# Kernel tuning notes

Hardware: AMD Instinct MI355X
Metric: run time of the kernel (lower is better)

## Reference

```python
import jax, jax.numpy as jnp
import numpy as np

B, T, C = 8, 1024, 1024
H, D = 16, 64  # num_heads, head_size

def setup_inputs() -> dict:
    key = jax.random.key(0)
    ks = jax.random.split(key, 6)
    s = C ** -0.5
    return {
        "x": jax.random.normal(ks[0], (B, T, C), dtype=jnp.float32),
        "Wq": jax.random.normal(ks[1], (H, C, D), dtype=jnp.float32) * s,
        "Wk": jax.random.normal(ks[2], (H, C, D), dtype=jnp.float32) * s,
        "Wv": jax.random.normal(ks[3], (H, C, D), dtype=jnp.float32) * s,
        "Wproj": jax.random.normal(ks[4], (H * D, C), dtype=jnp.float32) * ((H * D) ** -0.5),
        "bproj": jnp.zeros((C,), dtype=jnp.float32),
    }

def reference(x, Wq, Wk, Wv, Wproj, bproj):
    # per-head QKV projections, batched over heads via einsum (same math as looped heads)
    q = jnp.einsum('btc,hcd->bhtd', x, Wq)
    k = jnp.einsum('btc,hcd->bhtd', x, Wk)
    v = jnp.einsum('btc,hcd->bhtd', x, Wv)
    scale = D ** -0.5  # k.shape[-1]**-0.5 in original head
    scores = jnp.einsum('bhtd,bhsd->bhts', q, k) * scale  # [B,H,T,T]
    Tn = x.shape[1]
    causal = jnp.tril(jnp.ones((Tn, Tn), dtype=bool))
    scores = jnp.where(causal, scores, jnp.float32(-jnp.inf))
    att = jax.nn.softmax(scores, axis=-1)
    out = jnp.einsum('bhts,bhsd->bhtd', att, v)          # [B,H,T,D]
    out = out.transpose(0, 2, 1, 3).reshape(x.shape[0], Tn, H * D)  # concat heads
    return out @ Wproj + bproj  # dropout is identity at p=0.0
```

## Files before the change

### kernel.cpp

```cpp
#include <hip/hip_runtime.h>
#include <hip/hip_bf16.h>

#define B_ 8
#define T_ 1024
#define C_ 1024
#define H_ 16
#define D_ 64
#define QKVLD 3072

typedef short v4s __attribute__((ext_vector_type(4)));
typedef short v8s __attribute__((ext_vector_type(8)));
typedef float v4f __attribute__((ext_vector_type(4)));
typedef float v16f __attribute__((ext_vector_type(16)));

__device__ __forceinline__ unsigned short f2b(float f) {
    unsigned int u = __builtin_bit_cast(unsigned int, f);
    unsigned int lsb = (u >> 16) & 1u;
    u += 0x7fffu + lsb;
    return (unsigned short)(u >> 16);
}

__device__ __forceinline__ v4s pack4(float p0, float p1, float p2, float p3) {
    unsigned int a = (__builtin_bit_cast(unsigned int, p0) + 0x8000u) >> 16;
    unsigned int b = (__builtin_bit_cast(unsigned int, p1) + 0x8000u) & 0xFFFF0000u;
    unsigned int c = (__builtin_bit_cast(unsigned int, p2) + 0x8000u) >> 16;
    unsigned int d = (__builtin_bit_cast(unsigned int, p3) + 0x8000u) & 0xFFFF0000u;
    union { unsigned int u[2]; v4s v; } t;
    t.u[0] = a | b; t.u[1] = c | d;
    return t.v;
}

#define MFMA32(A, B, C) __builtin_amdgcn_mfma_f32_16x16x32_bf16(A, B, C, 0, 0, 0)
#define MFMA16(A, B, C) __builtin_amdgcn_mfma_f32_16x16x16bf16_1k(A, B, C, 0, 0, 0)

#define GLOAD16(gp, lp)                                                          \
    __builtin_amdgcn_global_load_lds(                                            \
        (const __attribute__((address_space(1))) unsigned int*)(gp),             \
        (__attribute__((address_space(3))) unsigned int*)(lp), 16, 0, 0)

__global__ void prep_kernel(const float* __restrict__ x, const float* __restrict__ Wq,
                            const float* __restrict__ Wk, const float* __restrict__ Wv,
                            const float* __restrict__ Wproj,
                            unsigned short* __restrict__ xb,
                            unsigned short* __restrict__ WqkvT,
                            unsigned short* __restrict__ WprojT) {
    __shared__ unsigned short t[64][65];
    int g = blockIdx.x;
    if (g < 8192) {
        int i = (g * 256 + (int)threadIdx.x) * 4;
        float4 v = *(const float4*)(x + i);
        ushort4 o;
        o.x = f2b(v.x); o.y = f2b(v.y); o.z = f2b(v.z); o.w = f2b(v.w);
        *(ushort4*)(xb + i) = o;
    } else if (g < 8192 + 768) {
        int idx = g - 8192;
        int z = idx >> 4;
        int h = z / 3, part = z % 3;
        const float* src = (part == 0 ? Wq : (part == 1 ? Wk : Wv)) + (size_t)h * C_ * D_;
        int c0 = (idx & 15) * 64;
        for (int i = threadIdx.x; i < 4096; i += 256) {
            int r = i >> 6, d = i & 63;
            t[d][r] = f2b(src[(size_t)(c0 + r) * D_ + d]);
        }
        __syncthreads();
        unsigned short* dst = WqkvT + (size_t)(part * 1024 + h * 64) * C_;
        for (int i = threadIdx.x; i < 4096; i += 256) {
            int d = i >> 6, r = i & 63;
            dst[(size_t)d * C_ + c0 + r] = t[d][r];
        }
    } else {
        int idx = g - 8960;
        int n0 = (idx & 15) * 64, k0 = (idx >> 4) * 64;
        for (int i = threadIdx.x; i < 4096; i += 256) {
            int r = i >> 6, c = i & 63;
            t[c][r] = f2b(Wproj[(size_t)(k0 + r) * C_ + n0 + c]);
        }
        __syncthreads();
        for (int i = threadIdx.x; i < 4096; i += 256) {
            int n = i >> 6, k = i & 63;
            WprojT[(size_t)(n0 + n) * 1024 + k0 + k] = t[n][k];
        }
    }
}

__global__ __launch_bounds__(256, 2) void gemm_qkv(const unsigned short* __restrict__ A,
                                                   const unsigned short* __restrict__ Bt,
                                                   unsigned short* __restrict__ Cout,
                                                   unsigned short* __restrict__ Vt,
                                                   int K, int ldc) {
    __shared__ unsigned short smem[24576];

    int tid = threadIdx.x;
    int lane = tid & 63, w = tid >> 6;
    int half = lane >> 5, l32 = lane & 31;
    int wm = w >> 1, wn = w & 1;
    int g = blockIdx.x;
    int xcd = g & 7;
    int bank = g >> 3;
    int j = g >> 4;

    if ((bank & 1) == 0) {
        constexpr int ABUF = 256 * 32;
        constexpr int BBUF = 128 * 32;
        unsigned short* lA0 = smem;
        unsigned short* lB0 = smem + 2 * ABUF;

        int m0 = (xcd * 4 + (j & 3)) * 256;
        int n0 = (j >> 2) * 128;

        const unsigned short* gA[4];
        int offA[4];
        #pragma unroll
        for (int jj = 0; jj < 4; jj++) {
            int c = jj * 256 + tid;
            int row = c >> 2;
            int col8 = ((c & 3) ^ ((row >> 1) & 3)) * 8;
            gA[jj] = A + (size_t)(m0 + row) * K + col8;
            offA[jj] = (jj * 256 + w * 64) * 16;
        }
        const unsigned short* gB[2];
        int offB[2];
        #pragma unroll
        for (int jj = 0; jj < 2; jj++) {
            int c = jj * 256 + tid;
            int row = c >> 2;
            int col8 = ((c & 3) ^ ((row >> 1) & 3)) * 8;
            gB[jj] = Bt + (size_t)(n0 + row) * K + col8;
            offB[jj] = (jj * 256 + w * 64) * 16;
        }

        int am[4], bn[2];
        #pragma unroll
        for (int mi = 0; mi < 4; mi++) am[mi] = wm * 128 + mi * 32 + l32;
        #pragma unroll
        for (int ni = 0; ni < 2; ni++) bn[ni] = wn * 64 + ni * 32 + l32;

        v16f acc[4][2];
        #pragma unroll
        for (int mi = 0; mi < 4; mi++)
            #pragma unroll
            for (int ni = 0; ni < 2; ni++)
                #pragma unroll
                for (int r = 0; r < 16; r++) acc[mi][ni][r] = 0.f;

        int ktiles = K >> 5;
        #pragma unroll
        for (int jj = 0; jj < 4; jj++) GLOAD16(gA[jj], (char*)lA0 + offA[jj]);
        #pragma unroll
        for (int jj = 0; jj < 2; jj++) GLOAD16(gB[jj], (char*)lB0 + offB[jj]);

        for (int it = 0; it < ktiles; it++) {
            int cur = it & 1, nxt = cur ^ 1;
            __asm__ volatile("s_waitcnt vmcnt(0)" ::: "memory");
            __asm__ volatile("s_barrier" ::: "memory");
            {
                int kn = (it + 1 < ktiles) ? (it + 1) * 32 : it * 32;
                #pragma unroll
                for (int jj = 0; jj < 4; jj++) GLOAD16(gA[jj] + kn, (char*)(lA0 + nxt * ABUF) + offA[jj]);
                #pragma unroll
                for (int jj = 0; jj < 2; jj++) GLOAD16(gB[jj] + kn, (char*)(lB0 + nxt * BBUF) + offB[jj]);
            }
            const unsigned short* bufA = lA0 + cur * ABUF;
            const unsigned short* bufB = lB0 + cur * BBUF;
            #pragma unroll
            for (int step = 0; step < 2; step++) {
                int gc = step * 2 + half;
                v8s af[4], bf[2];
                #pragma unroll
                for (int mi = 0; mi < 4; mi++)
                    af[mi] = *(const v8s*)&bufA[am[mi] * 32 + ((gc ^ ((am[mi] >> 1) & 3)) * 8)];
                #pragma unroll
                for (int ni = 0; ni < 2; ni++)
                    bf[ni] = *(const v8s*)&bufB[bn[ni] * 32 + ((gc ^ ((bn[ni] >> 1) & 3)) * 8)];
                #pragma unroll
                for (int mi = 0; mi < 4; mi++)
                    #pragma unroll
                    for (int ni = 0; ni < 2; ni++)
                        acc[mi][ni] = __builtin_amdgcn_mfma_f32_32x32x16_bf16(af[mi], bf[ni], acc[mi][ni], 0, 0, 0);
            }
        }
        float scl = (n0 >= 1024) ? 0.125f : 1.0f;
        #pragma unroll
        for (int mi = 0; mi < 4; mi++) {
            #pragma unroll
            for (int ni = 0; ni < 2; ni++) {
                int col = n0 + wn * 64 + ni * 32 + l32;
                #pragma unroll
                for (int r = 0; r < 16; r++) {
                    int row = m0 + wm * 128 + mi * 32 + (r & 3) + 8 * (r >> 2) + 4 * half;
                    Cout[(size_t)row * ldc + col] = f2b(acc[mi][ni][r] * scl);
                }
            }
        }
    } else {
        constexpr int ABUF = 128 * 32;
        constexpr int BBUF = 128 * 32;
        unsigned short* lA = smem;
        unsigned short* lB = smem + 3 * ABUF;

        const unsigned short* Bv = Bt + (size_t)2048 * K;
        int m0 = (xcd * 8 + (j & 7)) * 128;
        int n0 = (j >> 3) * 128;

        const unsigned short* gA[2];
        int offA[2];
        #pragma unroll
        for (int jj = 0; jj < 2; jj++) {
            int c = jj * 256 + tid;
            int row = c >> 2;
            int col8 = ((c & 3) ^ ((row >> 1) & 3)) * 8;
            gA[jj] = A + (size_t)(m0 + row) * K + col8;
            offA[jj] = (jj * 256 + w * 64) * 16;
        }
        const unsigned short* gB[2];
        int offB[2];
        #pragma unroll
        for (int jj = 0; jj < 2; jj++) {
            int c = jj * 256 + tid;
            int row = c >> 2;
            int col8 = ((c & 3) ^ ((row >> 1) & 3)) * 8;
            gB[jj] = Bv + (size_t)(n0 + row) * K + col8;
            offB[jj] = (jj * 256 + w * 64) * 16;
        }

        int am[2], bn[2];
        #pragma unroll
        for (int mi = 0; mi < 2; mi++) am[mi] = wm * 64 + mi * 32 + l32;
        #pragma unroll
        for (int ni = 0; ni < 2; ni++) bn[ni] = wn * 64 + ni * 32 + l32;

        v16f acc[2][2];
        #pragma unroll
        for (int mi = 0; mi < 2; mi++)
            #pragma unroll
            for (int ni = 0; ni < 2; ni++)
                #pragma unroll
                for (int r = 0; r < 16; r++) acc[mi][ni][r] = 0.f;

        int kt = K >> 5;
        #pragma unroll
        for (int jj = 0; jj < 2; jj++) GLOAD16(gA[jj], (char*)lA + offA[jj]);
        #pragma unroll
        for (int jj = 0; jj < 2; jj++) GLOAD16(gB[jj], (char*)lB + offB[jj]);
        #pragma unroll
        for (int jj = 0; jj < 2; jj++) GLOAD16(gA[jj] + 32, (char*)(lA + ABUF) + offA[jj]);
        #pragma unroll
        for (int jj = 0; jj < 2; jj++) GLOAD16(gB[jj] + 32, (char*)(lB + BBUF) + offB[jj]);

        int cur = 0;
        for (int it = 0; it < kt; it++) {
            int nx2 = cur + 2; if (nx2 >= 3) nx2 -= 3;
            __asm__ volatile("s_waitcnt vmcnt(4)" ::: "memory");
            __asm__ volatile("s_barrier" ::: "memory");
            {
                int kn = ((it + 2 < kt) ? it + 2 : kt - 1) << 5;
                #pragma unroll
                for (int jj = 0; jj < 2; jj++) GLOAD16(gA[jj] + kn, (char*)(lA + nx2 * ABUF) + offA[jj]);
                #pragma unroll
                for (int jj = 0; jj < 2; jj++) GLOAD16(gB[jj] + kn, (char*)(lB + nx2 * BBUF) + offB[jj]);
            }
            const unsigned short* bufA = lA + cur * ABUF;
            const unsigned short* bufB = lB + cur * BBUF;
            #pragma unroll
            for (int step = 0; step < 2; step++) {
                int gch = step * 2 + half;
                v8s af[2], bf[2];
                #pragma unroll
                for (int mi = 0; mi < 2; mi++)
                    af[mi] = *(const v8s*)&bufA[am[mi] * 32 + ((gch ^ ((am[mi] >> 1) & 3)) * 8)];
                #pragma unroll
                for (int ni = 0; ni < 2; ni++)
                    bf[ni] = *(const v8s*)&bufB[bn[ni] * 32 + ((gch ^ ((bn[ni] >> 1) & 3)) * 8)];
                #pragma unroll
                for (int mi = 0; mi < 2; mi++)
                    #pragma unroll
                    for (int ni = 0; ni < 2; ni++)
                        acc[mi][ni] = __builtin_amdgcn_mfma_f32_32x32x16_bf16(af[mi], bf[ni], acc[mi][ni], 0, 0, 0);
            }
            cur = cur + 1; if (cur >= 3) cur -= 3;
        }
        unsigned short* sT = lA;
        int bB = m0 >> 10;
        int t0 = m0 & 1023;
        #pragma unroll
        for (int p = 0; p < 2; p++) {
            __syncthreads();
            if (wn == p) {
                #pragma unroll
                for (int mi = 0; mi < 2; mi++)
                    #pragma unroll
                    for (int ni = 0; ni < 2; ni++) {
                        int cl = ni * 32 + l32;
                        #pragma unroll
                        for (int r = 0; r < 16; r++) {
                            int rowl = wm * 64 + mi * 32 + (r & 3) + 8 * (r >> 2) + 4 * half;
                            sT[cl * 136 + rowl] = f2b(acc[mi][ni][r]);
                        }
                    }
            }
            __syncthreads();
            #pragma unroll
            for (int jj = 0; jj < 4; jj++) {
                int c = jj * 256 + tid;
                int cl = c >> 4, ch = c & 15;
                int vcol = n0 + p * 64 + cl;
                int hh = vcol >> 6, dd = vcol & 63;
                *(v8s*)&Vt[(((size_t)bB * 16 + hh) * 64 + dd) * T_ + t0 + ch * 8] =
                    *(const v8s*)&sT[cl * 136 + ch * 8];
            }
        }
    }
}

__global__ __launch_bounds__(256, 3) void gemm_proj(const unsigned short* __restrict__ A,
                                                    const unsigned short* __restrict__ Bt,
                                                    float* __restrict__ Cout,
                                                    const float* __restrict__ bias,
                                                    int M, int N, int K) {
    constexpr int ABUF = 128 * 32;
    constexpr int BBUF = 128 * 32;
    __shared__ unsigned short lA[3 * ABUF];
    __shared__ unsigned short lB[3 * BBUF];

    int tid = threadIdx.x;
    int lane = tid & 63, w = tid >> 6;
    int half = lane >> 5, l32 = lane & 31;
    int wm = w >> 1, wn = w & 1;

    int g = blockIdx.x;
    int nbm = M / 128;
    int stripe = nbm >> 3;
    int xcd = g & 7, s = g >> 3;
    int m0 = (xcd * stripe + (s % stripe)) * 128;
    int n0 = (s / stripe) * 128;

    const unsigned short* gA[2];
    int offA[2];
    #pragma unroll
    for (int j = 0; j < 2; j++) {
        int c = j * 256 + tid;
        int row = c >> 2;
        int col8 = ((c & 3) ^ ((row >> 1) & 3)) * 8;
        gA[j] = A + (size_t)(m0 + row) * K + col8;
        offA[j] = (j * 256 + w * 64) * 16;
    }
    const unsigned short* gB[2];
    int offB[2];
    #pragma unroll
    for (int j = 0; j < 2; j++) {
        int c = j * 256 + tid;
        int row = c >> 2;
        int col8 = ((c & 3) ^ ((row >> 1) & 3)) * 8;
        gB[j] = Bt + (size_t)(n0 + row) * K + col8;
        offB[j] = (j * 256 + w * 64) * 16;
    }

    int am[2], bn[2];
    #pragma unroll
    for (int mi = 0; mi < 2; mi++) am[mi] = wm * 64 + mi * 32 + l32;
    #pragma unroll
    for (int ni = 0; ni < 2; ni++) bn[ni] = wn * 64 + ni * 32 + l32;

    v16f acc[2][2];
    #pragma unroll
    for (int mi = 0; mi < 2; mi++)
        #pragma unroll
        for (int ni = 0; ni < 2; ni++)
            #pragma unroll
            for (int r = 0; r < 16; r++) acc[mi][ni][r] = 0.f;

    int kt = K >> 5;
    #pragma unroll
    for (int j = 0; j < 2; j++) GLOAD16(gA[j], (char*)lA + offA[j]);
    #pragma unroll
    for (int j = 0; j < 2; j++) GLOAD16(gB[j], (char*)lB + offB[j]);
    #pragma unroll
    for (int j = 0; j < 2; j++) GLOAD16(gA[j] + 32, (char*)(lA + ABUF) + offA[j]);
    #pragma unroll
    for (int j = 0; j < 2; j++) GLOAD16(gB[j] + 32, (char*)(lB + BBUF) + offB[j]);

    int cur = 0;
    for (int it = 0; it < kt; it++) {
        int nx2 = cur + 2; if (nx2 >= 3) nx2 -= 3;
        __asm__ volatile("s_waitcnt vmcnt(4)" ::: "memory");
        __asm__ volatile("s_barrier" ::: "memory");
        {
            int kn = ((it + 2 < kt) ? it + 2 : kt - 1) << 5;
            #pragma unroll
            for (int j = 0; j < 2; j++) GLOAD16(gA[j] + kn, (char*)(lA + nx2 * ABUF) + offA[j]);
            #pragma unroll
            for (int j = 0; j < 2; j++) GLOAD16(gB[j] + kn, (char*)(lB + nx2 * BBUF) + offB[j]);
        }
        const unsigned short* bufA = lA + cur * ABUF;
        const unsigned short* bufB = lB + cur * BBUF;
        #pragma unroll
        for (int step = 0; step < 2; step++) {
            int gch = step * 2 + half;
            v8s af[2], bf[2];
            #pragma unroll
            for (int mi = 0; mi < 2; mi++)
                af[mi] = *(const v8s*)&bufA[am[mi] * 32 + ((gch ^ ((am[mi] >> 1) & 3)) * 8)];
            #pragma unroll
            for (int ni = 0; ni < 2; ni++)
                bf[ni] = *(const v8s*)&bufB[bn[ni] * 32 + ((gch ^ ((bn[ni] >> 1) & 3)) * 8)];
            #pragma unroll
            for (int mi = 0; mi < 2; mi++)
                #pragma unroll
                for (int ni = 0; ni < 2; ni++)
                    acc[mi][ni] = __builtin_amdgcn_mfma_f32_32x32x16_bf16(af[mi], bf[ni], acc[mi][ni], 0, 0, 0);
        }
        cur = cur + 1; if (cur >= 3) cur -= 3;
    }
    #pragma unroll
    for (int mi = 0; mi < 2; mi++) {
        #pragma unroll
        for (int ni = 0; ni < 2; ni++) {
            int col = n0 + wn * 64 + ni * 32 + l32;
            #pragma unroll
            for (int r = 0; r < 16; r++) {
                int row = m0 + wm * 64 + mi * 32 + (r & 3) + 8 * (r >> 2) + 4 * half;
                Cout[(size_t)row * N + col] = acc[mi][ni][r] + bias[col];
            }
        }
    }
}

__global__ __launch_bounds__(256) void attn_kernel(const unsigned short* __restrict__ QKV,
                                                   const unsigned short* __restrict__ Vt,
                                                   unsigned short* __restrict__ Ob) {
    int bh = blockIdx.x;
    int qt = 15 - blockIdx.y;
    int b = bh >> 4, h = bh & 15;
    int tid = threadIdx.x, lane = tid & 63, w = tid >> 6;
    int quad = lane >> 4, l16 = lane & 15;
    int qg0 = qt * 64 + w * 16;

    __shared__ unsigned short lK[2][2][64][32];
    __shared__ unsigned short lV[2][2][64][32];

    v8s aq0, aq1;
    {
        const unsigned short* qp = QKV + (size_t)(b * T_ + qg0 + l16) * QKVLD + h * 64;
        aq0 = *(const v8s*)(qp + quad * 8);
        aq1 = *(const v8s*)(qp + 32 + quad * 8);
    }

    const unsigned short* gK[2];
    const unsigned short* gV[2];
    int ldsOff[2];
    #pragma unroll
    for (int j = 0; j < 2; j++) {
        int c = j * 256 + tid;
        int halfp = c >> 8, row = (c >> 2) & 63;
        int col8 = ((c & 3) ^ ((row >> 1) & 3)) * 8;
        gK[j] = QKV + (size_t)(b * T_ + row) * QKVLD + 1024 + h * 64 + halfp * 32 + col8;
        gV[j] = Vt + ((size_t)bh * 64 + row) * T_ + halfp * 32 + col8;
        ldsOff[j] = (j * 256 + w * 64) * 16;
    }
    int rcol = (quad ^ ((l16 >> 1) & 3)) * 8;

    v4f accO[4];
    float lsum = 0.f;
    #pragma unroll
    for (int i = 0; i < 4; i++) accO[i] = (v4f){0.f, 0.f, 0.f, 0.f};

    int ntiles = qt + 1;

    #pragma unroll
    for (int j = 0; j < 2; j++) GLOAD16(gK[j], (char*)&lK[0][0][0][0] + ldsOff[j]);
    #pragma unroll
    for (int j = 0; j < 2; j++) GLOAD16(gV[j], (char*)&lV[0][0][0][0] + ldsOff[j]);

    for (int it = 0; it < ntiles; it++) {
        int cur = it & 1, nxt = cur ^ 1;
        int s0 = it * 64;
        __asm__ volatile("s_waitcnt vmcnt(0)" ::: "memory");
        __asm__ volatile("s_barrier" ::: "memory");
        {
            int itn = (it + 1 < ntiles) ? it + 1 : it;
            size_t koff = (size_t)itn * 64 * QKVLD;
            #pragma unroll
            for (int j = 0; j < 2; j++)
                GLOAD16(gK[j] + koff, (char*)&lK[nxt][0][0][0] + ldsOff[j]);
            size_t voff = (size_t)itn * 64;
            #pragma unroll
            for (int j = 0; j < 2; j++)
                GLOAD16(gV[j] + voff, (char*)&lV[nxt][0][0][0] + ldsOff[j]);
        }
        v4f sf[4];
        #pragma unroll
        for (int nt = 0; nt < 4; nt++) {
            v8s bk0 = *(const v8s*)&lK[cur][0][nt * 16 + l16][rcol];
            v8s bk1 = *(const v8s*)&lK[cur][1][nt * 16 + l16][rcol];
            v4f a = (v4f){0.f, 0.f, 0.f, 0.f};
            a = MFMA32(bk0, aq0, a);
            a = MFMA32(bk1, aq1, a);
            sf[nt] = a;
        }
        bool diag = (it == ntiles - 1);
        int qg = qg0 + l16;
        v4s pP[4];
        #pragma unroll
        for (int nt = 0; nt < 4; nt++) {
            float p[4];
            #pragma unroll
            for (int r = 0; r < 4; r++) {
                float e = __expf(sf[nt][r]);
                if (diag) {
                    int sg = s0 + nt * 16 + quad * 4 + r;
                    e = (sg > qg) ? 0.f : e;
                }
                p[r] = e;
                lsum += e;
            }
            pP[nt] = pack4(p[0], p[1], p[2], p[3]);
        }
        #pragma unroll
        for (int kb = 0; kb < 4; kb++) {
            int sc_ = kb >> 1;
            int ccg = (kb & 1) * 2 + (quad >> 1);
            #pragma unroll
            for (int dt = 0; dt < 4; dt++) {
                int d = dt * 16 + l16;
                int ccp = ccg ^ ((l16 >> 1) & 3);
                v4s bv = *(const v4s*)&lV[cur][sc_][d][ccp * 8 + (quad & 1) * 4];
                accO[dt] = MFMA16(pP[kb], bv, accO[dt]);
            }
        }
    }
    float ls = lsum;
    ls += __shfl_xor(ls, 16, 64);
    ls += __shfl_xor(ls, 32, 64);
    #pragma unroll
    for (int r = 0; r < 4; r++) {
        float lq = __shfl(ls, quad * 4 + r, 64);
        float inv = 1.0f / lq;
        int q = qg0 + quad * 4 + r;
        #pragma unroll
        for (int dt = 0; dt < 4; dt++) {
            int d = dt * 16 + l16;
            Ob[(size_t)(b * T_ + q) * (H_ * D_) + h * 64 + d] = f2b(accO[dt][r] * inv);
        }
    }
}

extern "C" void kernel_launch(void* const* d_in, const int* in_sizes, int n_in,
                              void* d_out, int out_size, void* d_ws, size_t ws_size,
                              hipStream_t stream) {
    const float* x     = (const float*)d_in[0];
    const float* Wq    = (const float*)d_in[1];
    const float* Wk    = (const float*)d_in[2];
    const float* Wv    = (const float*)d_in[3];
    const float* Wproj = (const float*)d_in[4];
    const float* bproj = (const float*)d_in[5];
    float* out = (float*)d_out;

    char* ws = (char*)d_ws;
    unsigned short* xb     = (unsigned short*)ws;
    unsigned short* WqkvT  = (unsigned short*)(ws + 16777216);
    unsigned short* WprojT = (unsigned short*)(ws + 23068672);
    unsigned short* QKV    = (unsigned short*)(ws + 25165824);
    unsigned short* Vt     = (unsigned short*)(ws + 75497472);
    unsigned short* Ob     = (unsigned short*)(ws + 92274688);

    prep_kernel<<<dim3(9216), dim3(256), 0, stream>>>(x, Wq, Wk, Wv, Wproj, xb, WqkvT, WprojT);
    gemm_qkv<<<dim3(1024), dim3(256), 0, stream>>>(xb, WqkvT, QKV, Vt, 1024, QKVLD);
    attn_kernel<<<dim3(128, 16), dim3(256), 0, stream>>>(QKV, Vt, Ob);
    gemm_proj<<<dim3(512), dim3(256), 0, stream>>>(Ob, WprojT, out, bproj, 8192, 1024, 1024);
}
```

Baseline: 230.9 us.

## Process 128 query rows per attention block to reuse K/V tiles across two subtiles

Each attention workgroup now handles 128 query rows instead of 64, with each wave computing two 16-row subtiles that share the same K and V fragments read from LDS. This halves the grid along the query axis and halves the global K/V traffic and LDS reads per query row. In exchange it raises register pressure (two accumulator sets), lowers block count and parallelism, and wastes some work on the two diagonal tiles where masking now spans a wider region.

```diff
diff --git a/kernel.cpp b/kernel.cpp
--- a/kernel.cpp
+++ b/kernel.cpp
@@ -429,20 +429,21 @@
                                                    const unsigned short* __restrict__ Vt,
                                                    unsigned short* __restrict__ Ob) {
     int bh = blockIdx.x;
-    int qt = 15 - blockIdx.y;
+    int qt = 7 - blockIdx.y;
     int b = bh >> 4, h = bh & 15;
     int tid = threadIdx.x, lane = tid & 63, w = tid >> 6;
     int quad = lane >> 4, l16 = lane & 15;
-    int qg0 = qt * 64 + w * 16;
+    int qg0 = qt * 128 + w * 32;
 
     __shared__ unsigned short lK[2][2][64][32];
     __shared__ unsigned short lV[2][2][64][32];
 
-    v8s aq0, aq1;
-    {
-        const unsigned short* qp = QKV + (size_t)(b * T_ + qg0 + l16) * QKVLD + h * 64;
-        aq0 = *(const v8s*)(qp + quad * 8);
-        aq1 = *(const v8s*)(qp + 32 + quad * 8);
+    v8s aq[2][2];
+    #pragma unroll
+    for (int st = 0; st < 2; st++) {
+        const unsigned short* qp = QKV + (size_t)(b * T_ + qg0 + st * 16 + l16) * QKVLD + h * 64;
+        aq[st][0] = *(const v8s*)(qp + quad * 8);
+        aq[st][1] = *(const v8s*)(qp + 32 + quad * 8);
     }
 
     const unsigned short* gK[2];
@@ -459,12 +460,14 @@
     }
     int rcol = (quad ^ ((l16 >> 1) & 3)) * 8;
 
-    v4f accO[4];
-    float lsum = 0.f;
-    #pragma unroll
-    for (int i = 0; i < 4; i++) accO[i] = (v4f){0.f, 0.f, 0.f, 0.f};
-
-    int ntiles = qt + 1;
+    v4f accO[2][4];
+    float lsum[2] = {0.f, 0.f};
+    #pragma unroll
+    for (int st = 0; st < 2; st++)
+        #pragma unroll
+        for (int i = 0; i < 4; i++) accO[st][i] = (v4f){0.f, 0.f, 0.f, 0.f};
+
+    int ntiles = 2 * qt + 2;
 
     #pragma unroll
     for (int j = 0; j < 2; j++) GLOAD16(gK[j], (char*)&lK[0][0][0][0] + ldsOff[j]);
@@ -487,33 +490,31 @@
             for (int j = 0; j < 2; j++)
                 GLOAD16(gV[j] + voff, (char*)&lV[nxt][0][0][0] + ldsOff[j]);
         }
-        v4f sf[4];
+        bool diag = (it >= ntiles - 2);
+        v4s pP[2][4];
         #pragma unroll
         for (int nt = 0; nt < 4; nt++) {
             v8s bk0 = *(const v8s*)&lK[cur][0][nt * 16 + l16][rcol];
             v8s bk1 = *(const v8s*)&lK[cur][1][nt * 16 + l16][rcol];
-            v4f a = (v4f){0.f, 0.f, 0.f, 0.f};
-            a = MFMA32(bk0, aq0, a);
-            a = MFMA32(bk1, aq1, a);
-            sf[nt] = a;
-        }
-        bool diag = (it == ntiles - 1);
-        int qg = qg0 + l16;
-        v4s pP[4];
-        #pragma unroll
-        for (int nt = 0; nt < 4; nt++) {
-            float p[4];
-            #pragma unroll
-            for (int r = 0; r < 4; r++) {
-                float e = __expf(sf[nt][r]);
-                if (diag) {
-                    int sg = s0 + nt * 16 + quad * 4 + r;
-                    e = (sg > qg) ? 0.f : e;
+            #pragma unroll
+            for (int st = 0; st < 2; st++) {
+                v4f a = (v4f){0.f, 0.f, 0.f, 0.f};
+                a = MFMA32(bk0, aq[st][0], a);
+                a = MFMA32(bk1, aq[st][1], a);
+                int qg = qg0 + st * 16 + l16;
+                float p[4];
+                #pragma unroll
+                for (int r = 0; r < 4; r++) {
+                    float e = __expf(a[r]);
+                    if (diag) {
+                        int sg = s0 + nt * 16 + quad * 4 + r;
+                        e = (sg > qg) ? 0.f : e;
+                    }
+                    p[r] = e;
+                    lsum[st] += e;
                 }
-                p[r] = e;
-                lsum += e;
-            }
-            pP[nt] = pack4(p[0], p[1], p[2], p[3]);
+                pP[st][nt] = pack4(p[0], p[1], p[2], p[3]);
+            }
         }
         #pragma unroll
         for (int kb = 0; kb < 4; kb++) {
@@ -524,22 +525,26 @@
                 int d = dt * 16 + l16;
                 int ccp = ccg ^ ((l16 >> 1) & 3);
                 v4s bv = *(const v4s*)&lV[cur][sc_][d][ccp * 8 + (quad & 1) * 4];
-                accO[dt] = MFMA16(pP[kb], bv, accO[dt]);
-            }
-        }
-    }
-    float ls = lsum;
-    ls += __shfl_xor(ls, 16, 64);
-    ls += __shfl_xor(ls, 32, 64);
-    #pragma unroll
-    for (int r = 0; r < 4; r++) {
-        float lq = __shfl(ls, quad * 4 + r, 64);
-        float inv = 1.0f / lq;
-        int q = qg0 + quad * 4 + r;
-        #pragma unroll
-        for (int dt = 0; dt < 4; dt++) {
-            int d = dt * 16 + l16;
-            Ob[(size_t)(b * T_ + q) * (H_ * D_) + h * 64 + d] = f2b(accO[dt][r] * inv);
+                accO[0][dt] = MFMA16(pP[0][kb], bv, accO[0][dt]);
+                accO[1][dt] = MFMA16(pP[1][kb], bv, accO[1][dt]);
+            }
+        }
+    }
+    #pragma unroll
+    for (int st = 0; st < 2; st++) {
+        float ls = lsum[st];
+        ls += __shfl_xor(ls, 16, 64);
+        ls += __shfl_xor(ls, 32, 64);
+        #pragma unroll
+        for (int r = 0; r < 4; r++) {
+            float lq = __shfl(ls, quad * 4 + r, 64);
+            float inv = 1.0f / lq;
+            int q = qg0 + st * 16 + quad * 4 + r;
+            #pragma unroll
+            for (int dt = 0; dt < 4; dt++) {
+                int d = dt * 16 + l16;
+                Ob[(size_t)(b * T_ + q) * (H_ * D_) + h * 64 + d] = f2b(accO[st][dt][r] * inv);
+            }
         }
     }
 }
@@ -565,6 +570,6 @@
 
     prep_kernel<<<dim3(9216), dim3(256), 0, stream>>>(x, Wq, Wk, Wv, Wproj, xb, WqkvT, WprojT);
     gemm_qkv<<<dim3(1024), dim3(256), 0, stream>>>(xb, WqkvT, QKV, Vt, 1024, QKVLD);
-    attn_kernel<<<dim3(128, 16), dim3(256), 0, stream>>>(QKV, Vt, Ob);
+    attn_kernel<<<dim3(128, 8), dim3(256), 0, stream>>>(QKV, Vt, Ob);
     gemm_proj<<<dim3(512), dim3(256), 0, stream>>>(Ob, WprojT, out, bproj, 8192, 1024, 1024);
 }
```

After: 230.3 us. No clear change (-0.3%).
